# Performance work log

Measured on AMD Instinct MI355X. Metric: run time of the kernel, lower is better.

The kernel has to match this reference:

```python
import jax, jax.numpy as jnp
from jax import lax
import numpy as np

DIM = 48
HEADS = 2
HIDDEN = 96  # int(dim * 2.0)
EPS_LN = 1e-5
EPS_NORM = 1e-12


def _ln(x, w, b):
    # WithBias LayerNorm over channel dim (dim=1 in NCHW == last dim in b,(hw),c)
    mu = jnp.mean(x, axis=1, keepdims=True)
    var = jnp.var(x, axis=1, keepdims=True)
    return (x - mu) / jnp.sqrt(var + EPS_LN) * w[None, :, None, None] + b[None, :, None, None]


def _conv1x1(x, w, b):
    # w: [O, C, 1, 1]
    return jnp.einsum('bchw,oc->bohw', x, w[:, :, 0, 0]) + b[None, :, None, None]


def _dwconv3(x, w, b):
    # w: [C, 1, 3, 3], groups=C
    y = lax.conv_general_dilated(x, w, (1, 1), 'SAME',
                                 feature_group_count=x.shape[1],
                                 dimension_numbers=('NCHW', 'OIHW', 'NCHW'))
    return y + b[None, :, None, None]


def _l2norm(x):
    n = jnp.sqrt(jnp.sum(x * x, axis=-1, keepdims=True))
    return x / jnp.maximum(n, EPS_NORM)


def setup_inputs() -> dict:
    key = jax.random.key(0)
    ks = jax.random.split(key, 12)
    s = 0.02
    inp = {
        'x': jax.random.normal(ks[0], (2, DIM, 64, 64), jnp.float32),
        'norm1_w': jnp.ones((DIM,), jnp.float32),
        'norm1_b': jnp.zeros((DIM,), jnp.float32),
        'qkv_w': jax.random.normal(ks[1], (DIM * 3, DIM, 1, 1), jnp.float32) * s,
        'qkv_b': jnp.zeros((DIM * 3,), jnp.float32),
        'qkvdw_w': jax.random.normal(ks[2], (DIM * 3, 1, 3, 3), jnp.float32) * s,
        'qkvdw_b': jnp.zeros((DIM * 3,), jnp.float32),
        'temperature': jnp.ones((HEADS, 1, 1), jnp.float32),
        'proj_w': jax.random.normal(ks[3], (DIM, DIM, 1, 1), jnp.float32) * s,
        'proj_b': jnp.zeros((DIM,), jnp.float32),
        'norm2_w': jnp.ones((DIM,), jnp.float32),
        'norm2_b': jnp.zeros((DIM,), jnp.float32),
        'fi_w': jax.random.normal(ks[4], (HIDDEN * 2, DIM, 1, 1), jnp.float32) * s,
        'fi_b': jnp.zeros((HIDDEN * 2,), jnp.float32),
        'fdw_w': jax.random.normal(ks[5], (HIDDEN * 2, 1, 3, 3), jnp.float32) * s,
        'fdw_b': jnp.zeros((HIDDEN * 2,), jnp.float32),
        'fo_w': jax.random.normal(ks[6], (DIM, HIDDEN, 1, 1), jnp.float32) * s,
        'fo_b': jnp.zeros((DIM,), jnp.float32),
    }
    return inp


def _block(x, norm1_w, norm1_b, qkv_w, qkv_b, qkvdw_w, qkvdw_b, temperature,
           proj_w, proj_b, norm2_w, norm2_b, fi_w, fi_b, fdw_w, fdw_b, fo_w, fo_b):
    b, c, h, w = x.shape
    n = h * w
    chead = c // HEADS
    # --- attention branch ---
    xn = _ln(x, norm1_w, norm1_b)
    qkv = _dwconv3(_conv1x1(xn, qkv_w, qkv_b), qkvdw_w, qkvdw_b)
    q, k, v = jnp.split(qkv, 3, axis=1)
    def to_heads(t):  # [b, heads*chead, h, w] -> [b, heads, n, chead]
        return t.reshape(b, HEADS, chead, n).transpose(0, 1, 3, 2)
    q, k, v = to_heads(q), to_heads(k), to_heads(v)
    q = _l2norm(q)
    k = _l2norm(k)
    attn = jnp.einsum('bhnc,bhmc->bhnm', q, k) * temperature[None]
    attn = jax.nn.softmax(attn, axis=-1)
    out = jnp.einsum('bhnm,bhmc->bhnc', attn, v)
    out = out.transpose(0, 1, 3, 2).reshape(b, c, h, w)
    x = x + _conv1x1(out, proj_w, proj_b)
    # --- ffn branch ---
    xn = _ln(x, norm2_w, norm2_b)
    y = _dwconv3(_conv1x1(xn, fi_w, fi_b), fdw_w, fdw_b)
    y1, y2 = jnp.split(y, 2, axis=1)
    y = jax.nn.gelu(y1, approximate=False) * y2
    x = x + _conv1x1(y, fo_w, fo_b)
    return x


def reference(x, norm1_w, norm1_b, qkv_w, qkv_b, qkvdw_w, qkvdw_b, temperature,
              proj_w, proj_b, norm2_w, norm2_b, fi_w, fi_b, fdw_w, fdw_b, fo_w, fo_b):
    return _block(x, norm1_w, norm1_b, qkv_w, qkv_b, qkvdw_w, qkvdw_b, temperature,
                  proj_w, proj_b, norm2_w, norm2_b, fi_w, fi_b, fdw_w, fdw_b, fo_w, fo_b)
```

## Files before the change

### kernel.cpp

```cpp
#include <hip/hip_runtime.h>
#include <hip/hip_bf16.h>
#include <math.h>

#define NPIX 4096
#define DIMC 48
#define NB 2
#define SPLIT 8

typedef __attribute__((ext_vector_type(8))) short short8;
typedef __attribute__((ext_vector_type(4))) float floatx4;

static __device__ inline short f2bf(float f) {
    union { float f; unsigned u; } v; v.f = f;
    unsigned r = (v.u + 0x7FFFu + ((v.u >> 16) & 1u)) >> 16;
    return (short)r;
}

__global__ void k_prepw(const float* __restrict__ qkvw, const float* __restrict__ fiw,
                        const float* __restrict__ fow, const float* __restrict__ projw,
                        short* __restrict__ qkvwbf, short* __restrict__ fiwbf,
                        short* __restrict__ fowbf, short* __restrict__ projwbf) {
    int idx = blockIdx.x * 256 + threadIdx.x;
    if (idx < 144 * 64) {
        int o = idx >> 6, c = idx & 63;
        qkvwbf[idx] = (c < 48) ? f2bf(qkvw[o * 48 + c]) : (short)0;
        return;
    }
    idx -= 144 * 64;
    if (idx < 192 * 64) {
        int o = idx >> 6, c = idx & 63;
        fiwbf[idx] = (c < 48) ? f2bf(fiw[o * 48 + c]) : (short)0;
        return;
    }
    idx -= 192 * 64;
    if (idx < 48 * 96) {
        fowbf[idx] = f2bf(fow[idx]);
        return;
    }
    idx -= 48 * 96;
    if (idx < 48 * 64) {
        int o = idx >> 6, c = idx & 63;
        projwbf[idx] = (c < 48) ? f2bf(projw[o * 48 + c]) : (short)0;
    }
}

__global__ __launch_bounds__(256) void k_attnpre(
    const float* __restrict__ x, const float* __restrict__ lw, const float* __restrict__ lb,
    const short* __restrict__ qkvwbf, const float* __restrict__ cb,
    const float* __restrict__ dww, const float* __restrict__ dwb,
    const float* __restrict__ temp,
    short* __restrict__ Qbf, short* __restrict__ Kbf, short* __restrict__ Vbf)
{
    int ox = blockIdx.x * 8, oy = blockIdx.y * 2, b = blockIdx.z;
    int t = threadIdx.x;
    int w = t >> 6, lane = t & 63, l15 = lane & 15, quad = lane >> 4;

    __shared__ short xnbf[48][72];
    __shared__ float fp[48][148];
    __shared__ float q2[16][148];

    if (t < 48) {
        float v[48];
        if (t < 40) {
            int gx = ox + (t % 10) - 1, gy = oy + (t / 10) - 1;
            if ((unsigned)gx < 64u && (unsigned)gy < 64u) {
                int p = gy * 64 + gx;
                const float* xb = x + (size_t)b * DIMC * NPIX;
                float mu = 0.f;
#pragma unroll
                for (int c = 0; c < 48; c++) { v[c] = xb[c * NPIX + p]; mu += v[c]; }
                mu *= (1.f / 48.f);
                float var = 0.f;
#pragma unroll
                for (int c = 0; c < 48; c++) { float d = v[c] - mu; var += d * d; }
                var *= (1.f / 48.f);
                float rs = rsqrtf(var + 1e-5f);
#pragma unroll
                for (int c = 0; c < 48; c++) v[c] = (v[c] - mu) * rs * lw[c] + lb[c];
            } else {
#pragma unroll
                for (int c = 0; c < 48; c++) v[c] = 0.f;
            }
        } else {
#pragma unroll
            for (int c = 0; c < 48; c++) v[c] = 0.f;
        }
        unsigned* row = (unsigned*)&xnbf[t][0];
#pragma unroll
        for (int i = 0; i < 24; i++) {
            __hip_bfloat162 pk = __float22bfloat162_rn(make_float2(v[2 * i], v[2 * i + 1]));
            row[i] = *(unsigned*)&pk;
        }
#pragma unroll
        for (int i = 24; i < 36; i++) row[i] = 0u;
    }
    __syncthreads();
    floatx4 zf = {0.f, 0.f, 0.f, 0.f};
    for (int job = w; job < 27; job += 4) {
        int pt = job / 9, ot = job % 9;
        short8 a0 = *(const short8*)&xnbf[pt * 16 + l15][quad * 8];
        short8 a1 = *(const short8*)&xnbf[pt * 16 + l15][32 + quad * 8];
        const short* wb = qkvwbf + (ot * 16 + l15) * 64;
        short8 b0 = *(const short8*)(wb + quad * 8);
        short8 b1 = *(const short8*)(wb + 32 + quad * 8);
        floatx4 c = __builtin_amdgcn_mfma_f32_16x16x32_bf16(a0, b0, zf, 0, 0, 0);
        c = __builtin_amdgcn_mfma_f32_16x16x32_bf16(a1, b1, c, 0, 0, 0);
        float bi = cb[ot * 16 + l15];
#pragma unroll
        for (int r = 0; r < 4; r++) {
            int hp = pt * 16 + quad * 4 + r;
            if (hp < 40) {
                int gx = ox + hp % 10 - 1, gy = oy + hp / 10 - 1;
                bool valid = (unsigned)gx < 64u && (unsigned)gy < 64u;
                fp[hp][ot * 16 + l15] = valid ? (c[r] + bi) : 0.f;
            }
        }
    }
    __syncthreads();
    for (int task = t; task < 16 * 144; task += 256) {
        int c = task % 144, px = task / 144;
        int hr = (px >> 3) * 10 + (px & 7) + 11;
        const float* wp = dww + (size_t)c * 9;
        float acc = dwb[c];
        acc += fp[hr - 11][c] * wp[0] + fp[hr - 10][c] * wp[1] + fp[hr - 9][c] * wp[2]
             + fp[hr - 1][c]  * wp[3] + fp[hr][c]      * wp[4] + fp[hr + 1][c] * wp[5]
             + fp[hr + 9][c]  * wp[6] + fp[hr + 10][c] * wp[7] + fp[hr + 11][c] * wp[8];
        q2[px][c] = acc;
    }
    __syncthreads();
    if (t < 32) {
        int px = t & 15, h = t >> 4;
        int ix = px & 7, iy = px >> 3;
        int n = (oy + iy) * 64 + ox + ix;
        int bh = b * 2 + h;
        float q[24], k[24], vv[24]; float sq = 0.f, sk = 0.f;
#pragma unroll
        for (int c = 0; c < 24; c++) {
            q[c] = q2[px][h * 24 + c];       sq += q[c] * q[c];
            k[c] = q2[px][48 + h * 24 + c];  sk += k[c] * k[c];
            vv[c] = q2[px][96 + h * 24 + c];
        }
        float rq = temp[h] / fmaxf(sqrtf(sq), 1e-12f);
        float rk = 1.f / fmaxf(sqrtf(sk), 1e-12f);
        short qs[32], ks[32];
#pragma unroll
        for (int c = 0; c < 24; c++) { qs[c] = f2bf(q[c] * rq); ks[c] = f2bf(k[c] * rk); }
#pragma unroll
        for (int c = 24; c < 32; c++) { qs[c] = 0; ks[c] = 0; }
        size_t ro = ((size_t)bh * NPIX + n) * 32;
#pragma unroll
        for (int i = 0; i < 4; i++) {
            short8 a, bb;
#pragma unroll
            for (int j = 0; j < 8; j++) { a[j] = qs[i * 8 + j]; bb[j] = ks[i * 8 + j]; }
            *(short8*)(Qbf + ro + i * 8) = a;
            *(short8*)(Kbf + ro + i * 8) = bb;
        }
        int r5 = n & 31;
        int vcol = (n & ~31) + ((r5 & 15) * 2 + (r5 >> 4));
#pragma unroll
        for (int c = 0; c < 24; c++)
            Vbf[((size_t)bh * 32 + c) * NPIX + vcol] = f2bf(vv[c]);
#pragma unroll
        for (int c = 24; c < 32; c++)
            Vbf[((size_t)bh * 32 + c) * NPIX + vcol] = 0;
    }
}

__global__ __launch_bounds__(256) void k_attn_mfma(const short* __restrict__ Qbf,
                                                   const short* __restrict__ Kbf,
                                                   const short* __restrict__ Vbf,
                                                   float* __restrict__ Opart,
                                                   float* __restrict__ lpart) {
    int qt = blockIdx.x, s = blockIdx.y, bh = blockIdx.z;
    int t = threadIdx.x;
    int w = t >> 6, lane = t & 63, l15 = lane & 15, quad = lane >> 4;

    __shared__ short tileK[2][32][40];
    __shared__ short tileV[2][32][40];
    __shared__ short P[4][16][40];

    int qrow0 = qt * 64 + w * 16;
    short8 aq = *(const short8*)(Qbf + ((size_t)bh * NPIX + qrow0 + l15) * 32 + quad * 8);

    int i = t & 127;
    int rr = i >> 2, qh = i & 3;
    bool isV = t >= 128;
    const short* srcK = Kbf + ((size_t)bh * NPIX + rr) * 32 + qh * 8;
    const short* srcV = Vbf + ((size_t)(bh * 32 + rr)) * NPIX + qh * 8;
    int dstoff = rr * 40 + qh * 8;

    int key0 = s * (NPIX / SPLIT);
    {
        short8 ld = isV ? *(const short8*)(srcV + key0)
                        : *(const short8*)(srcK + (size_t)key0 * 32);
        short* dst = (isV ? &tileV[0][0][0] : &tileK[0][0][0]) + dstoff;
        *(short8*)dst = ld;
    }

    floatx4 zf = {0.f, 0.f, 0.f, 0.f};
    floatx4 o0 = zf, o1 = zf;
    float ls[4] = {0.f, 0.f, 0.f, 0.f};

    const int NKT = (NPIX / SPLIT) / 32;
    for (int kt = 0; kt < NKT; kt++) {
        __syncthreads();
        int cur = kt & 1;
        short8 ld = {};
        if (kt < NKT - 1) {
            int kabs = key0 + (kt + 1) * 32;
            ld = isV ? *(const short8*)(srcV + kabs)
                     : *(const short8*)(srcK + (size_t)kabs * 32);
        }
        short8 b0  = *(const short8*)&tileK[cur][l15][quad * 8];
        short8 b1  = *(const short8*)&tileK[cur][l15 + 16][quad * 8];
        short8 vb0 = *(const short8*)&tileV[cur][l15][quad * 8];
        short8 vb1 = *(const short8*)&tileV[cur][l15 + 16][quad * 8];
        floatx4 s0 = __builtin_amdgcn_mfma_f32_16x16x32_bf16(aq, b0, zf, 0, 0, 0);
        floatx4 s1 = __builtin_amdgcn_mfma_f32_16x16x32_bf16(aq, b1, zf, 0, 0, 0);
#pragma unroll
        for (int r = 0; r < 4; r++) {
            float p0 = __expf(s0[r]);
            float p1 = __expf(s1[r]);
            ls[r] += p0 + p1;
            __hip_bfloat162 pk = __float22bfloat162_rn(make_float2(p0, p1));
            *(unsigned*)&P[w][quad * 4 + r][l15 * 2] = *(unsigned*)&pk;
        }
        short8 ap = *(const short8*)&P[w][l15][quad * 8];
        o0 = __builtin_amdgcn_mfma_f32_16x16x32_bf16(ap, vb0, o0, 0, 0, 0);
        o1 = __builtin_amdgcn_mfma_f32_16x16x32_bf16(ap, vb1, o1, 0, 0, 0);
        if (kt < NKT - 1) {
            short* dst = (isV ? &tileV[1 - cur][0][0] : &tileK[1 - cur][0][0]) + dstoff;
            *(short8*)dst = ld;
        }
    }
#pragma unroll
    for (int m = 1; m < 16; m <<= 1) {
#pragma unroll
        for (int r = 0; r < 4; r++) ls[r] += __shfl_xor(ls[r], m, 64);
    }
#pragma unroll
    for (int r = 0; r < 4; r++) {
        int n = qrow0 + quad * 4 + r;
        size_t base = (size_t)(bh * SPLIT + s) * 32;
        Opart[(base + l15) * NPIX + n] = o0[r];
        Opart[(base + 16 + l15) * NPIX + n] = o1[r];
        if (l15 == 0) lpart[((size_t)(bh * SPLIT + s)) * NPIX + n] = ls[r];
    }
}

__global__ __launch_bounds__(256) void k_projred(
    const float* __restrict__ x, const float* __restrict__ Opart,
    const float* __restrict__ lpart, const short* __restrict__ projwbf,
    const float* __restrict__ bias, float* __restrict__ x1)
{
    int px0 = blockIdx.x * 32;
    int b = blockIdx.y;
    int t = threadIdx.x;
    int w = t >> 6, lane = t & 63, l15 = lane & 15, quad = lane >> 4;

    __shared__ __align__(16) short Ash[32][72];
    __shared__ float rlsh[2][32];

    if (t < 64) {
        int h = t >> 5, px = t & 31;
        float l = 0.f;
#pragma unroll
        for (int s = 0; s < SPLIT; s++)
            l += lpart[((size_t)((b * 2 + h) * SPLIT + s)) * NPIX + px0 + px];
        rlsh[h][px] = 1.f / l;
    }
    {
        int px = t & 31, j = t >> 5;
        *(unsigned*)&Ash[px][48 + j * 2] = 0u;
    }
    __syncthreads();
#pragma unroll
    for (int pi = 0; pi < 6; pi++) {
        int idx = pi * 256 + t;
        int px = idx & 31, c = idx >> 5;
        int h = c / 24, ch = c % 24;
        float acc = 0.f;
#pragma unroll
        for (int s = 0; s < SPLIT; s++)
            acc += Opart[(((size_t)((b * 2 + h) * SPLIT + s)) * 32 + ch) * NPIX + px0 + px];
        Ash[px][c] = f2bf(acc * rlsh[h][px]);
    }
    __syncthreads();
    floatx4 zf = {0.f, 0.f, 0.f, 0.f};
    for (int job = w; job < 6; job += 4) {
        int pt = job / 3, ot = job % 3;
        short8 a0 = *(const short8*)&Ash[pt * 16 + l15][quad * 8];
        short8 a1 = *(const short8*)&Ash[pt * 16 + l15][32 + quad * 8];
        const short* wb = projwbf + (ot * 16 + l15) * 64;
        short8 b0 = *(const short8*)(wb + quad * 8);
        short8 b1 = *(const short8*)(wb + 32 + quad * 8);
        floatx4 c = __builtin_amdgcn_mfma_f32_16x16x32_bf16(a0, b0, zf, 0, 0, 0);
        c = __builtin_amdgcn_mfma_f32_16x16x32_bf16(a1, b1, c, 0, 0, 0);
        int oc = ot * 16 + l15;
        float bi = bias[oc];
#pragma unroll
        for (int r = 0; r < 4; r++) {
            int n = px0 + pt * 16 + quad * 4 + r;
            size_t idx = ((size_t)b * 48 + oc) * NPIX + n;
            x1[idx] = x[idx] + c[r] + bi;
        }
    }
}

__global__ __launch_bounds__(256) void k_ffn(
    const float* __restrict__ x1, const float* __restrict__ lw, const float* __restrict__ lb,
    const short* __restrict__ fiwbf, const float* __restrict__ fib,
    const float* __restrict__ fdww, const float* __restrict__ fdwb,
    const short* __restrict__ fowbf, const float* __restrict__ fob,
    float* __restrict__ out)
{
    int ox = blockIdx.x * 8, oy = blockIdx.y * 2, b = blockIdx.z;
    int t = threadIdx.x;
    int w = t >> 6, lane = t & 63, l15 = lane & 15, quad = lane >> 4;

    __shared__ short xnbf[48][72];
    __shared__ float fp[48][196];
    __shared__ short yv[16][104];

    if (t < 48) {
        float v[48];
        if (t < 40) {
            int gx = ox + (t % 10) - 1, gy = oy + (t / 10) - 1;
            if ((unsigned)gx < 64u && (unsigned)gy < 64u) {
                int p = gy * 64 + gx;
                const float* xb = x1 + (size_t)b * DIMC * NPIX;
                float mu = 0.f;
#pragma unroll
                for (int c = 0; c < 48; c++) { v[c] = xb[c * NPIX + p]; mu += v[c]; }
                mu *= (1.f / 48.f);
                float var = 0.f;
#pragma unroll
                for (int c = 0; c < 48; c++) { float d = v[c] - mu; var += d * d; }
                var *= (1.f / 48.f);
                float rs = rsqrtf(var + 1e-5f);
#pragma unroll
                for (int c = 0; c < 48; c++) v[c] = (v[c] - mu) * rs * lw[c] + lb[c];
            } else {
#pragma unroll
                for (int c = 0; c < 48; c++) v[c] = 0.f;
            }
        } else {
#pragma unroll
            for (int c = 0; c < 48; c++) v[c] = 0.f;
        }
        unsigned* row = (unsigned*)&xnbf[t][0];
#pragma unroll
        for (int i = 0; i < 24; i++) {
            __hip_bfloat162 pk = __float22bfloat162_rn(make_float2(v[2 * i], v[2 * i + 1]));
            row[i] = *(unsigned*)&pk;
        }
#pragma unroll
        for (int i = 24; i < 36; i++) row[i] = 0u;
    }
    __syncthreads();
    floatx4 zf = {0.f, 0.f, 0.f, 0.f};
    for (int job = w; job < 36; job += 4) {
        int pt = job / 12, ot = job % 12;
        short8 a0 = *(const short8*)&xnbf[pt * 16 + l15][quad * 8];
        short8 a1 = *(const short8*)&xnbf[pt * 16 + l15][32 + quad * 8];
        const short* wb = fiwbf + (ot * 16 + l15) * 64;
        short8 b0 = *(const short8*)(wb + quad * 8);
        short8 b1 = *(const short8*)(wb + 32 + quad * 8);
        floatx4 c = __builtin_amdgcn_mfma_f32_16x16x32_bf16(a0, b0, zf, 0, 0, 0);
        c = __builtin_amdgcn_mfma_f32_16x16x32_bf16(a1, b1, c, 0, 0, 0);
        float bi = fib[ot * 16 + l15];
#pragma unroll
        for (int r = 0; r < 4; r++) {
            int hp = pt * 16 + quad * 4 + r;
            if (hp < 40) {
                int gx = ox + hp % 10 - 1, gy = oy + hp / 10 - 1;
                bool valid = (unsigned)gx < 64u && (unsigned)gy < 64u;
                fp[hp][ot * 16 + l15] = valid ? (c[r] + bi) : 0.f;
            }
        }
    }
    __syncthreads();
    for (int task = t; task < 16 * 96; task += 256) {
        int c = task % 96, px = task / 96;
        int hr = (px >> 3) * 10 + (px & 7) + 11;
        const float* wp = fdww + (size_t)c * 9;
        float a = fdwb[c];
        a += fp[hr - 11][c] * wp[0] + fp[hr - 10][c] * wp[1] + fp[hr - 9][c] * wp[2]
           + fp[hr - 1][c]  * wp[3] + fp[hr][c]      * wp[4] + fp[hr + 1][c] * wp[5]
           + fp[hr + 9][c]  * wp[6] + fp[hr + 10][c] * wp[7] + fp[hr + 11][c] * wp[8];
        int c2 = c + 96;
        const float* wp2 = fdww + (size_t)c2 * 9;
        float g2 = fdwb[c2];
        g2 += fp[hr - 11][c2] * wp2[0] + fp[hr - 10][c2] * wp2[1] + fp[hr - 9][c2] * wp2[2]
            + fp[hr - 1][c2]  * wp2[3] + fp[hr][c2]      * wp2[4] + fp[hr + 1][c2] * wp2[5]
            + fp[hr + 9][c2]  * wp2[6] + fp[hr + 10][c2] * wp2[7] + fp[hr + 11][c2] * wp2[8];
        float ge = 0.5f * a * (1.f + erff(a * 0.70710678118654752f));
        yv[px][c] = f2bf(ge * g2);
    }
    __syncthreads();
    if (w < 3) {
        int ot = w;
        floatx4 c = zf;
#pragma unroll
        for (int k = 0; k < 3; k++) {
            short8 a = *(const short8*)&yv[l15][k * 32 + quad * 8];
            short8 bb = *(const short8*)(fowbf + (ot * 16 + l15) * 96 + k * 32 + quad * 8);
            c = __builtin_amdgcn_mfma_f32_16x16x32_bf16(a, bb, c, 0, 0, 0);
        }
        int oc = ot * 16 + l15;
        float bi = fob[oc];
#pragma unroll
        for (int r = 0; r < 4; r++) {
            int px = quad * 4 + r;
            int n = (oy + (px >> 3)) * 64 + ox + (px & 7);
            size_t idx = ((size_t)b * 48 + oc) * NPIX + n;
            out[idx] = x1[idx] + c[r] + bi;
        }
    }
}

extern "C" void kernel_launch(void* const* d_in, const int* in_sizes, int n_in,
                              void* d_out, int out_size, void* d_ws, size_t ws_size,
                              hipStream_t stream) {
    const float* x       = (const float*)d_in[0];
    const float* n1w     = (const float*)d_in[1];
    const float* n1b     = (const float*)d_in[2];
    const float* qkv_w   = (const float*)d_in[3];
    const float* qkv_b   = (const float*)d_in[4];
    const float* qkvdw_w = (const float*)d_in[5];
    const float* qkvdw_b = (const float*)d_in[6];
    const float* temp    = (const float*)d_in[7];
    const float* proj_w  = (const float*)d_in[8];
    const float* proj_b  = (const float*)d_in[9];
    const float* n2w     = (const float*)d_in[10];
    const float* n2b     = (const float*)d_in[11];
    const float* fi_w    = (const float*)d_in[12];
    const float* fi_b    = (const float*)d_in[13];
    const float* fdw_w   = (const float*)d_in[14];
    const float* fdw_b   = (const float*)d_in[15];
    const float* fo_w    = (const float*)d_in[16];
    const float* fo_b    = (const float*)d_in[17];

    float* ws = (float*)d_ws;
    short* Qbf   = (short*)ws;
    short* Kbf   = Qbf + 524288;
    short* Vbf   = Kbf + 524288;
    float* Opart = ws + 786432;
    float* lpart = Opart + 4194304;
    float* x1    = lpart + 131072;
    short* qkvwbf = (short*)(x1 + 393216);
    short* fiwbf  = qkvwbf + 9216;
    short* fowbf  = fiwbf + 12288;
    short* projwbf = fowbf + 4608;

    {
        int total = 144 * 64 + 192 * 64 + 48 * 96 + 48 * 64;
        k_prepw<<<(total + 255) / 256, 256, 0, stream>>>(qkv_w, fi_w, fo_w, proj_w,
                                                         qkvwbf, fiwbf, fowbf, projwbf);
    }
    {
        dim3 g(8, 32, NB);
        k_attnpre<<<g, 256, 0, stream>>>(x, n1w, n1b, qkvwbf, qkv_b, qkvdw_w, qkvdw_b,
                                         temp, Qbf, Kbf, Vbf);
    }
    {
        dim3 g(64, SPLIT, 4);
        k_attn_mfma<<<g, 256, 0, stream>>>(Qbf, Kbf, Vbf, Opart, lpart);
    }
    {
        dim3 g(128, NB);
        k_projred<<<g, 256, 0, stream>>>(x, Opart, lpart, projwbf, proj_b, x1);
    }
    {
        dim3 g(8, 32, NB);
        k_ffn<<<g, 256, 0, stream>>>(x1, n2w, n2b, fiwbf, fi_b, fdw_w, fdw_b,
                                     fowbf, fo_b, (float*)d_out);
    }
}
```

Before: 158.5 us.

## Split fused LN+conv+dwconv kernels into separate conv and depthwise stages

Splits the fused attention-prep and FFN kernels into two stages each. The first is an LN plus 1x1 conv MFMA kernel that writes bf16 pre-activations to global memory. The second is a depthwise-3x3 kernel that reads neighbours from global, which removes the halo recomputation of LN and the 1x1 conv, and the single-thread-heavy LN loop. The attention split factor also drops from 8 to 4. This costs extra kernel launches and a global round trip through bf16 intermediates, and the rounding to bf16 before the depthwise conv adds precision loss.

After: 167.9 us. +5.9%, slower.

```diff
diff --git a/kernel.cpp b/kernel.cpp
--- a/kernel.cpp
+++ b/kernel.cpp
@@ -5,15 +5,39 @@
 #define NPIX 4096
 #define DIMC 48
 #define NB 2
-#define SPLIT 8
+#define SPLIT 4
 
 typedef __attribute__((ext_vector_type(8))) short short8;
+typedef __attribute__((ext_vector_type(4))) short short4s;
 typedef __attribute__((ext_vector_type(4))) float floatx4;
 
 static __device__ inline short f2bf(float f) {
     union { float f; unsigned u; } v; v.f = f;
     unsigned r = (v.u + 0x7FFFu + ((v.u >> 16) & 1u)) >> 16;
     return (short)r;
+}
+static __device__ inline float bf2f(short s) {
+    union { unsigned u; float f; } v;
+    v.u = ((unsigned)(unsigned short)s) << 16;
+    return v.f;
+}
+
+static __device__ inline float dw3_at(const short* __restrict__ ip,
+                                      const float* __restrict__ wp,
+                                      int gx, int y, float acc) {
+#pragma unroll
+    for (int dy = -1; dy <= 1; dy++) {
+        int yy = y + dy;
+        if ((unsigned)yy < 64u) {
+#pragma unroll
+            for (int dx = -1; dx <= 1; dx++) {
+                int xx = gx + dx;
+                if ((unsigned)xx < 64u)
+                    acc += bf2f(ip[yy * 64 + xx]) * wp[(dy + 1) * 3 + (dx + 1)];
+            }
+        }
+    }
+    return acc;
 }
 
 __global__ void k_prepw(const float* __restrict__ qkvw, const float* __restrict__ fiw,
@@ -44,104 +68,102 @@
     }
 }
 
-__global__ __launch_bounds__(256) void k_attnpre(
-    const float* __restrict__ x, const float* __restrict__ lw, const float* __restrict__ lb,
-    const short* __restrict__ qkvwbf, const float* __restrict__ cb,
-    const float* __restrict__ dww, const float* __restrict__ dwb,
-    const float* __restrict__ temp,
-    short* __restrict__ Qbf, short* __restrict__ Kbf, short* __restrict__ Vbf)
+__global__ __launch_bounds__(256) void k_ln_conv_mfma(
+    const float* __restrict__ xin, const float* __restrict__ lw, const float* __restrict__ lb,
+    const short* __restrict__ wbf, const float* __restrict__ cb,
+    short* __restrict__ outbf, int OC)
 {
-    int ox = blockIdx.x * 8, oy = blockIdx.y * 2, b = blockIdx.z;
+    int px0 = blockIdx.x * 32;
+    int b = blockIdx.y;
     int t = threadIdx.x;
     int w = t >> 6, lane = t & 63, l15 = lane & 15, quad = lane >> 4;
 
-    __shared__ short xnbf[48][72];
-    __shared__ float fp[48][148];
-    __shared__ float q2[16][148];
-
-    if (t < 48) {
-        float v[48];
-        if (t < 40) {
-            int gx = ox + (t % 10) - 1, gy = oy + (t / 10) - 1;
-            if ((unsigned)gx < 64u && (unsigned)gy < 64u) {
-                int p = gy * 64 + gx;
-                const float* xb = x + (size_t)b * DIMC * NPIX;
-                float mu = 0.f;
-#pragma unroll
-                for (int c = 0; c < 48; c++) { v[c] = xb[c * NPIX + p]; mu += v[c]; }
-                mu *= (1.f / 48.f);
-                float var = 0.f;
-#pragma unroll
-                for (int c = 0; c < 48; c++) { float d = v[c] - mu; var += d * d; }
-                var *= (1.f / 48.f);
-                float rs = rsqrtf(var + 1e-5f);
-#pragma unroll
-                for (int c = 0; c < 48; c++) v[c] = (v[c] - mu) * rs * lw[c] + lb[c];
-            } else {
-#pragma unroll
-                for (int c = 0; c < 48; c++) v[c] = 0.f;
-            }
-        } else {
-#pragma unroll
-            for (int c = 0; c < 48; c++) v[c] = 0.f;
-        }
-        unsigned* row = (unsigned*)&xnbf[t][0];
-#pragma unroll
-        for (int i = 0; i < 24; i++) {
-            __hip_bfloat162 pk = __float22bfloat162_rn(make_float2(v[2 * i], v[2 * i + 1]));
-            row[i] = *(unsigned*)&pk;
-        }
-#pragma unroll
-        for (int i = 24; i < 36; i++) row[i] = 0u;
+    __shared__ float psum[8][32], psq[8][32];
+    __shared__ float muS[32], rsS[32];
+    __shared__ short xnbf[32][72];
+
+    int px = t & 31, g = t >> 5;
+    *(unsigned*)&xnbf[px][48 + g * 2] = 0u;
+
+    float v[6];
+    float s = 0.f, sq = 0.f;
+#pragma unroll
+    for (int i = 0; i < 6; i++) {
+        v[i] = xin[((size_t)b * 48 + g * 6 + i) * (size_t)NPIX + px0 + px];
+        s += v[i]; sq += v[i] * v[i];
+    }
+    psum[g][px] = s; psq[g][px] = sq;
+    __syncthreads();
+    if (t < 32) {
+        float ss = 0.f, qq = 0.f;
+#pragma unroll
+        for (int i = 0; i < 8; i++) { ss += psum[i][t]; qq += psq[i][t]; }
+        float mu = ss * (1.f / 48.f);
+        float var = qq * (1.f / 48.f) - mu * mu;
+        muS[t] = mu; rsS[t] = rsqrtf(var + 1e-5f);
+    }
+    __syncthreads();
+    {
+        float mu = muS[px], rs = rsS[px];
+#pragma unroll
+        for (int i = 0; i < 6; i++) {
+            int c = g * 6 + i;
+            xnbf[px][c] = f2bf((v[i] - mu) * rs * lw[c] + lb[c]);
+        }
     }
     __syncthreads();
     floatx4 zf = {0.f, 0.f, 0.f, 0.f};
-    for (int job = w; job < 27; job += 4) {
-        int pt = job / 9, ot = job % 9;
+    int oct = OC >> 4;
+    int njobs = 2 * oct;
+    for (int job = w; job < njobs; job += 4) {
+        int pt = job / oct, ot = job % oct;
         short8 a0 = *(const short8*)&xnbf[pt * 16 + l15][quad * 8];
         short8 a1 = *(const short8*)&xnbf[pt * 16 + l15][32 + quad * 8];
-        const short* wb = qkvwbf + (ot * 16 + l15) * 64;
+        const short* wb = wbf + (ot * 16 + l15) * 64;
         short8 b0 = *(const short8*)(wb + quad * 8);
         short8 b1 = *(const short8*)(wb + 32 + quad * 8);
         floatx4 c = __builtin_amdgcn_mfma_f32_16x16x32_bf16(a0, b0, zf, 0, 0, 0);
         c = __builtin_amdgcn_mfma_f32_16x16x32_bf16(a1, b1, c, 0, 0, 0);
-        float bi = cb[ot * 16 + l15];
-#pragma unroll
-        for (int r = 0; r < 4; r++) {
-            int hp = pt * 16 + quad * 4 + r;
-            if (hp < 40) {
-                int gx = ox + hp % 10 - 1, gy = oy + hp / 10 - 1;
-                bool valid = (unsigned)gx < 64u && (unsigned)gy < 64u;
-                fp[hp][ot * 16 + l15] = valid ? (c[r] + bi) : 0.f;
-            }
-        }
-    }
-    __syncthreads();
-    for (int task = t; task < 16 * 144; task += 256) {
-        int c = task % 144, px = task / 144;
-        int hr = (px >> 3) * 10 + (px & 7) + 11;
-        const float* wp = dww + (size_t)c * 9;
-        float acc = dwb[c];
-        acc += fp[hr - 11][c] * wp[0] + fp[hr - 10][c] * wp[1] + fp[hr - 9][c] * wp[2]
-             + fp[hr - 1][c]  * wp[3] + fp[hr][c]      * wp[4] + fp[hr + 1][c] * wp[5]
-             + fp[hr + 9][c]  * wp[6] + fp[hr + 10][c] * wp[7] + fp[hr + 11][c] * wp[8];
-        q2[px][c] = acc;
+        int oc = ot * 16 + l15;
+        float bi = cb[oc];
+        short4s st;
+#pragma unroll
+        for (int r = 0; r < 4; r++) st[r] = f2bf(c[r] + bi);
+        *(short4s*)(outbf + ((size_t)b * OC + oc) * (size_t)NPIX + px0 + pt * 16 + quad * 4) = st;
+    }
+}
+
+__global__ __launch_bounds__(256) void k_dw3heads(
+    const short* __restrict__ qkv_pre, const float* __restrict__ dww,
+    const float* __restrict__ dwb, const float* __restrict__ temp,
+    short* __restrict__ Qbf, short* __restrict__ Kbf, short* __restrict__ Vbf)
+{
+    int px0 = blockIdx.x * 16;
+    int y = blockIdx.y, b = blockIdx.z;
+    int t = threadIdx.x;
+    __shared__ float q2[16][148];
+
+    int px = t & 15, g = t >> 4;
+    int gx = px0 + px;
+    const short* base = qkv_pre + (size_t)b * 144 * NPIX;
+    for (int i = 0; i < 9; i++) {
+        int c = g * 9 + i;
+        q2[px][c] = dw3_at(base + (size_t)c * NPIX, dww + c * 9, gx, y, dwb[c]);
     }
     __syncthreads();
     if (t < 32) {
-        int px = t & 15, h = t >> 4;
-        int ix = px & 7, iy = px >> 3;
-        int n = (oy + iy) * 64 + ox + ix;
+        int hpx = t & 15, h = t >> 4;
+        int n = y * 64 + px0 + hpx;
         int bh = b * 2 + h;
-        float q[24], k[24], vv[24]; float sq = 0.f, sk = 0.f;
+        float q[24], k[24], vv[24]; float sqs = 0.f, sks = 0.f;
 #pragma unroll
         for (int c = 0; c < 24; c++) {
-            q[c] = q2[px][h * 24 + c];       sq += q[c] * q[c];
-            k[c] = q2[px][48 + h * 24 + c];  sk += k[c] * k[c];
-            vv[c] = q2[px][96 + h * 24 + c];
-        }
-        float rq = temp[h] / fmaxf(sqrtf(sq), 1e-12f);
-        float rk = 1.f / fmaxf(sqrtf(sk), 1e-12f);
+            q[c] = q2[hpx][h * 24 + c];       sqs += q[c] * q[c];
+            k[c] = q2[hpx][48 + h * 24 + c];  sks += k[c] * k[c];
+            vv[c] = q2[hpx][96 + h * 24 + c];
+        }
+        float rq = temp[h] / fmaxf(sqrtf(sqs), 1e-12f);
+        float rk = 1.f / fmaxf(sqrtf(sks), 1e-12f);
         short qs[32], ks[32];
 #pragma unroll
         for (int c = 0; c < 24; c++) { qs[c] = f2bf(q[c] * rq); ks[c] = f2bf(k[c] * rk); }
@@ -242,9 +264,9 @@
 #pragma unroll
     for (int r = 0; r < 4; r++) {
         int n = qrow0 + quad * 4 + r;
-        size_t base = (size_t)(bh * SPLIT + s) * 32;
-        Opart[(base + l15) * NPIX + n] = o0[r];
-        Opart[(base + 16 + l15) * NPIX + n] = o1[r];
+        size_t base2 = (size_t)(bh * SPLIT + s) * 32;
+        Opart[(base2 + l15) * NPIX + n] = o0[r];
+        Opart[(base2 + 16 + l15) * NPIX + n] = o1[r];
         if (l15 == 0) lpart[((size_t)(bh * SPLIT + s)) * NPIX + n] = ls[r];
     }
 }
@@ -308,112 +330,44 @@
     }
 }
 
-__global__ __launch_bounds__(256) void k_ffn(
-    const float* __restrict__ x1, const float* __restrict__ lw, const float* __restrict__ lb,
-    const short* __restrict__ fiwbf, const float* __restrict__ fib,
-    const float* __restrict__ fdww, const float* __restrict__ fdwb,
-    const short* __restrict__ fowbf, const float* __restrict__ fob,
+__global__ __launch_bounds__(256) void k_dwgatefo(
+    const short* __restrict__ fp_pre, const float* __restrict__ fdww,
+    const float* __restrict__ fdwb, const short* __restrict__ fowbf,
+    const float* __restrict__ fob, const float* __restrict__ x1,
     float* __restrict__ out)
 {
-    int ox = blockIdx.x * 8, oy = blockIdx.y * 2, b = blockIdx.z;
+    int px0 = blockIdx.x * 16;
+    int y = blockIdx.y, b = blockIdx.z;
     int t = threadIdx.x;
     int w = t >> 6, lane = t & 63, l15 = lane & 15, quad = lane >> 4;
 
-    __shared__ short xnbf[48][72];
-    __shared__ float fp[48][196];
     __shared__ short yv[16][104];
 
-    if (t < 48) {
-        float v[48];
-        if (t < 40) {
-            int gx = ox + (t % 10) - 1, gy = oy + (t / 10) - 1;
-            if ((unsigned)gx < 64u && (unsigned)gy < 64u) {
-                int p = gy * 64 + gx;
-                const float* xb = x1 + (size_t)b * DIMC * NPIX;
-                float mu = 0.f;
-#pragma unroll
-                for (int c = 0; c < 48; c++) { v[c] = xb[c * NPIX + p]; mu += v[c]; }
-                mu *= (1.f / 48.f);
-                float var = 0.f;
-#pragma unroll
-                for (int c = 0; c < 48; c++) { float d = v[c] - mu; var += d * d; }
-                var *= (1.f / 48.f);
-                float rs = rsqrtf(var + 1e-5f);
-#pragma unroll
-                for (int c = 0; c < 48; c++) v[c] = (v[c] - mu) * rs * lw[c] + lb[c];
-            } else {
-#pragma unroll
-                for (int c = 0; c < 48; c++) v[c] = 0.f;
-            }
-        } else {
-#pragma unroll
-            for (int c = 0; c < 48; c++) v[c] = 0.f;
-        }
-        unsigned* row = (unsigned*)&xnbf[t][0];
-#pragma unroll
-        for (int i = 0; i < 24; i++) {
-            __hip_bfloat162 pk = __float22bfloat162_rn(make_float2(v[2 * i], v[2 * i + 1]));
-            row[i] = *(unsigned*)&pk;
-        }
-#pragma unroll
-        for (int i = 24; i < 36; i++) row[i] = 0u;
-    }
-    __syncthreads();
-    floatx4 zf = {0.f, 0.f, 0.f, 0.f};
-    for (int job = w; job < 36; job += 4) {
-        int pt = job / 12, ot = job % 12;
-        short8 a0 = *(const short8*)&xnbf[pt * 16 + l15][quad * 8];
-        short8 a1 = *(const short8*)&xnbf[pt * 16 + l15][32 + quad * 8];
-        const short* wb = fiwbf + (ot * 16 + l15) * 64;
-        short8 b0 = *(const short8*)(wb + quad * 8);
-        short8 b1 = *(const short8*)(wb + 32 + quad * 8);
-        floatx4 c = __builtin_amdgcn_mfma_f32_16x16x32_bf16(a0, b0, zf, 0, 0, 0);
-        c = __builtin_amdgcn_mfma_f32_16x16x32_bf16(a1, b1, c, 0, 0, 0);
-        float bi = fib[ot * 16 + l15];
-#pragma unroll
-        for (int r = 0; r < 4; r++) {
-            int hp = pt * 16 + quad * 4 + r;
-            if (hp < 40) {
-                int gx = ox + hp % 10 - 1, gy = oy + hp / 10 - 1;
-                bool valid = (unsigned)gx < 64u && (unsigned)gy < 64u;
-                fp[hp][ot * 16 + l15] = valid ? (c[r] + bi) : 0.f;
-            }
-        }
-    }
-    __syncthreads();
-    for (int task = t; task < 16 * 96; task += 256) {
-        int c = task % 96, px = task / 96;
-        int hr = (px >> 3) * 10 + (px & 7) + 11;
-        const float* wp = fdww + (size_t)c * 9;
-        float a = fdwb[c];
-        a += fp[hr - 11][c] * wp[0] + fp[hr - 10][c] * wp[1] + fp[hr - 9][c] * wp[2]
-           + fp[hr - 1][c]  * wp[3] + fp[hr][c]      * wp[4] + fp[hr + 1][c] * wp[5]
-           + fp[hr + 9][c]  * wp[6] + fp[hr + 10][c] * wp[7] + fp[hr + 11][c] * wp[8];
+    int px = t & 15, g = t >> 4;
+    int gx = px0 + px;
+    const short* base = fp_pre + (size_t)b * 192 * NPIX;
+    for (int i = 0; i < 6; i++) {
+        int c = g * 6 + i;
+        float a  = dw3_at(base + (size_t)c * NPIX, fdww + c * 9, gx, y, fdwb[c]);
         int c2 = c + 96;
-        const float* wp2 = fdww + (size_t)c2 * 9;
-        float g2 = fdwb[c2];
-        g2 += fp[hr - 11][c2] * wp2[0] + fp[hr - 10][c2] * wp2[1] + fp[hr - 9][c2] * wp2[2]
-            + fp[hr - 1][c2]  * wp2[3] + fp[hr][c2]      * wp2[4] + fp[hr + 1][c2] * wp2[5]
-            + fp[hr + 9][c2]  * wp2[6] + fp[hr + 10][c2] * wp2[7] + fp[hr + 11][c2] * wp2[8];
+        float g2 = dw3_at(base + (size_t)c2 * NPIX, fdww + c2 * 9, gx, y, fdwb[c2]);
         float ge = 0.5f * a * (1.f + erff(a * 0.70710678118654752f));
         yv[px][c] = f2bf(ge * g2);
     }
     __syncthreads();
     if (w < 3) {
-        int ot = w;
-        floatx4 c = zf;
+        floatx4 c = {0.f, 0.f, 0.f, 0.f};
 #pragma unroll
         for (int k = 0; k < 3; k++) {
             short8 a = *(const short8*)&yv[l15][k * 32 + quad * 8];
-            short8 bb = *(const short8*)(fowbf + (ot * 16 + l15) * 96 + k * 32 + quad * 8);
+            short8 bb = *(const short8*)(fowbf + (w * 16 + l15) * 96 + k * 32 + quad * 8);
             c = __builtin_amdgcn_mfma_f32_16x16x32_bf16(a, bb, c, 0, 0, 0);
         }
-        int oc = ot * 16 + l15;
+        int oc = w * 16 + l15;
         float bi = fob[oc];
 #pragma unroll
         for (int r = 0; r < 4; r++) {
-            int px = quad * 4 + r;
-            int n = (oy + (px >> 3)) * 64 + ox + (px & 7);
+            int n = y * 64 + px0 + quad * 4 + r;
             size_t idx = ((size_t)b * 48 + oc) * NPIX + n;
             out[idx] = x1[idx] + c[r] + bi;
         }
@@ -443,15 +397,17 @@
     const float* fo_b    = (const float*)d_in[17];
 
     float* ws = (float*)d_ws;
-    short* Qbf   = (short*)ws;
-    short* Kbf   = Qbf + 524288;
-    short* Vbf   = Kbf + 524288;
-    float* Opart = ws + 786432;
-    float* lpart = Opart + 4194304;
-    float* x1    = lpart + 131072;
-    short* qkvwbf = (short*)(x1 + 393216);
-    short* fiwbf  = qkvwbf + 9216;
-    short* fowbf  = fiwbf + 12288;
+    short* qkv_pre = (short*)ws;
+    short* fp_pre  = (short*)(ws + 589824);
+    short* Qbf     = (short*)(ws + 1376256);
+    short* Kbf     = (short*)(ws + 1638400);
+    short* Vbf     = (short*)(ws + 1900544);
+    float* Opart   = ws + 2162688;
+    float* lpart   = ws + 4259840;
+    float* x1      = ws + 4325376;
+    short* qkvwbf  = (short*)(ws + 4718592);
+    short* fiwbf   = qkvwbf + 9216;
+    short* fowbf   = fiwbf + 12288;
     short* projwbf = fowbf + 4608;
 
     {
@@ -460,9 +416,12 @@
                                                          qkvwbf, fiwbf, fowbf, projwbf);
     }
     {
-        dim3 g(8, 32, NB);
-        k_attnpre<<<g, 256, 0, stream>>>(x, n1w, n1b, qkvwbf, qkv_b, qkvdw_w, qkvdw_b,
-                                         temp, Qbf, Kbf, Vbf);
+        dim3 g(128, NB);
+        k_ln_conv_mfma<<<g, 256, 0, stream>>>(x, n1w, n1b, qkvwbf, qkv_b, qkv_pre, 144);
+    }
+    {
+        dim3 g(4, 64, NB);
+        k_dw3heads<<<g, 256, 0, stream>>>(qkv_pre, qkvdw_w, qkvdw_b, temp, Qbf, Kbf, Vbf);
     }
     {
         dim3 g(64, SPLIT, 4);
@@ -473,8 +432,12 @@
         k_projred<<<g, 256, 0, stream>>>(x, Opart, lpart, projwbf, proj_b, x1);
     }
     {
-        dim3 g(8, 32, NB);
-        k_ffn<<<g, 256, 0, stream>>>(x1, n2w, n2b, fiwbf, fi_b, fdw_w, fdw_b,
-                                     fowbf, fo_b, (float*)d_out);
-    }
-}
+        dim3 g(128, NB);
+        k_ln_conv_mfma<<<g, 256, 0, stream>>>(x1, n2w, n2b, fiwbf, fi_b, fp_pre, 192);
+    }
+    {
+        dim3 g(4, 64, NB);
+        k_dwgatefo<<<g, 256, 0, stream>>>(fp_pre, fdw_w, fdw_b, fowbf, fo_b, x1,
+                                          (float*)d_out);
+    }
+}
```
